# Performance work log

Measured on AMD Instinct MI355X. Metric: run time of the kernel, lower is better.

## Reference

```python
import jax, jax.numpy as jnp
import numpy as np

COMMITMENT = 1.0


def setup_inputs() -> dict:
    key = jax.random.key(0)
    k1, k2 = jax.random.split(key)
    input = jax.random.normal(k1, (8, 64, 64, 256), dtype=jnp.float32)
    embed = jax.random.normal(k2, (256, 8192), dtype=jnp.float32)  # [dim, n_embed]
    return {"input": input, "embed": embed}


def reference(input, embed):
    dim = embed.shape[0]
    flatten = input.reshape(-1, dim)  # [N, dim]
    dist = (
        jnp.sum(flatten * flatten, axis=1, keepdims=True)
        - 2.0 * (flatten @ embed)
        + jnp.sum(embed * embed, axis=0, keepdims=True)
    )
    embed_ind = jnp.argmin(dist, axis=1)  # == (-dist).max(1) indices
    embed_ind = embed_ind.reshape(input.shape[:-1])  # [B, H, W]
    quantize = jnp.take(embed.T, embed_ind, axis=0)  # codebook lookup [B,H,W,dim]
    loss = jnp.mean((jax.lax.stop_gradient(quantize) - input) ** 2) * COMMITMENT
    quantize = input + jax.lax.stop_gradient(quantize - input)  # straight-through
    return quantize, embed_ind, loss
```

## Files before the change

kernel.cpp:

```cpp
#include <hip/hip_runtime.h>
#include <hip/hip_fp16.h>

#define NROW 32768
#define DIM  256
#define NC   8192
#define CAP  16384
#define MARGINF 0.375f
#define BIAS 512.0f
#define AST 576
#define BST 576
#define LOSS_SCALE (1.0f / 8388608.0f)

typedef __attribute__((ext_vector_type(8))) _Float16 half8;
typedef __attribute__((ext_vector_type(4))) _Float16 half4;
typedef __attribute__((ext_vector_type(4))) float   floatx4;
typedef const __attribute__((address_space(1))) void* gas_p;
typedef __attribute__((address_space(3))) void*       las_p;

static __device__ __forceinline__ unsigned short f2hb(float f) {
    _Float16 h = (_Float16)f;
    unsigned short u;
    __builtin_memcpy(&u, &h, 2);
    return u;
}
static __device__ __forceinline__ unsigned umin_(unsigned a, unsigned b) { return a < b ? a : b; }
static __device__ __forceinline__ unsigned umax_(unsigned a, unsigned b) { return a > b ? a : b; }


__global__ void prep_a_k(const float* __restrict__ x, unsigned short* __restrict__ Ah,
                         float* __restrict__ norms) {
    int row  = blockIdx.x * 4 + (threadIdx.x >> 6);
    int lane = threadIdx.x & 63;
    const float4 v = ((const float4*)(x + (size_t)row * DIM))[lane];
    float s = v.x * v.x + v.y * v.y + v.z * v.z + v.w * v.w;
#pragma unroll
    for (int off = 32; off; off >>= 1) s += __shfl_down(s, off, 64);
    if (lane == 0) norms[row] = s;
    ushort4 hi4 = make_ushort4(f2hb(v.x), f2hb(v.y), f2hb(v.z), f2hb(v.w));
    ushort4 lo4 = make_ushort4(f2hb(v.x - (float)(_Float16)v.x),
                               f2hb(v.y - (float)(_Float16)v.y),
                               f2hb(v.z - (float)(_Float16)v.z),
                               f2hb(v.w - (float)(_Float16)v.w));
    unsigned short* rp = Ah + (size_t)row * AST;
    *(ushort4*)(rp + lane * 4)       = hi4;
    *(ushort4*)(rp + 288 + lane * 4) = lo4;
    if (lane < 8) {
        ushort4 ob = make_ushort4(0, 0, 0, 0);
        if (lane == 0) { ob.x = 0x3C00; ob.y = 0x3C00; }
        *(ushort4*)(rp + 256 + lane * 4) = ob;
    }
}

__global__ void code_norms_k(const float* __restrict__ e, unsigned short* __restrict__ Bh,
                             float* __restrict__ cHalf) {
    int j = blockIdx.x * 256 + threadIdx.x;
    float s = 0.f;
    for (int d = 0; d < DIM; ++d) { float v = e[(size_t)d * NC + j]; s += v * v; }
    cHalf[j] = 0.5f * s;
    float t = -0.5f * s - BIAS;
    unsigned short hi = f2hb(t);
    _Float16 hf; __builtin_memcpy(&hf, &hi, 2);
    unsigned short lo = f2hb(t - (float)hf);
    unsigned short* p = Bh + (size_t)j * BST + 256;
    p[0] = hi; p[1] = lo;
    for (int k2 = 2; k2 < 32; ++k2) p[k2] = 0;
}

__global__ void prep_b_k(const float* __restrict__ e, unsigned short* __restrict__ Bh) {
    __shared__ float t[32][33];
    int jb = blockIdx.x * 32, db = blockIdx.y * 32;
#pragma unroll
    for (int i = 0; i < 4; ++i)
        t[threadIdx.y + i * 8][threadIdx.x] =
            e[(size_t)(db + threadIdx.y + i * 8) * NC + jb + threadIdx.x];
    __syncthreads();
#pragma unroll
    for (int i = 0; i < 4; ++i) {
        int j = jb + threadIdx.y + i * 8;
        int d = db + threadIdx.x;
        float val = t[threadIdx.x][threadIdx.y + i * 8];
        Bh[(size_t)j * BST + d]       = f2hb(val);
        Bh[(size_t)j * BST + 288 + d] = f2hb(val - (float)(_Float16)val);
    }
}


__global__ __launch_bounds__(256, 1) void vq_cheap_k(
    const unsigned short* __restrict__ Ah, const unsigned short* __restrict__ Bh,
    const float* __restrict__ cHalf,
    float* __restrict__ pv, int* __restrict__ pj, float* __restrict__ psv)
{
    __shared__ __align__(16) _Float16 Asl[8][4096];
    __shared__ __align__(16) _Float16 Bsl[2][8192];
    __shared__ float chl[2048];

    const int tid  = threadIdx.x;
    const int js   = blockIdx.x & 3;
    const int rb   = blockIdx.x >> 2;
    const int row0 = rb * 128, col0 = js * 2048;
    const int lane = tid & 63, l15 = lane & 15, lq = lane >> 4;
    const int wave = tid >> 6;
    const int wr = (wave >> 1) * 64;
    const int wc = (wave & 1) * 128;
    const int sr = tid >> 2, sp = (tid & 3) * 8;

    const unsigned short* Abase = Ah + (size_t)(row0 + sr) * AST + sp;
#pragma unroll
    for (int c = 0; c < 8; ++c) {
        __builtin_amdgcn_global_load_lds((gas_p)(Abase + c * 32),            (las_p)&Asl[c][tid * 8],        16, 0, 0);
        __builtin_amdgcn_global_load_lds((gas_p)(Abase + 64 * AST + c * 32), (las_p)&Asl[c][2048 + tid * 8], 16, 0, 0);
    }
    {
        const float4* cp = (const float4*)(cHalf + col0);
        float4 a = cp[tid * 2], b = cp[tid * 2 + 1];
        a.x += BIAS; a.y += BIAS; a.z += BIAS; a.w += BIAS;
        b.x += BIAS; b.y += BIAS; b.z += BIAS; b.w += BIAS;
        ((float4*)chl)[tid * 2]     = a;
        ((float4*)chl)[tid * 2 + 1] = b;
    }

#define LOADB(JT_, C_, BUF_)                                                                  \
    do {                                                                                      \
        const unsigned short* bb_ = Bh + (size_t)(col0 + (JT_) * 256 + sr) * BST + (C_) * 32 + sp; \
        _Float16* lb_ = &Bsl[(BUF_)][tid * 8];                                                \
        __builtin_amdgcn_global_load_lds((gas_p)(bb_),             (las_p)lb_,           16, 0, 0); \
        __builtin_amdgcn_global_load_lds((gas_p)(bb_ + 64 * BST),  (las_p)(lb_ + 2048),  16, 0, 0); \
        __builtin_amdgcn_global_load_lds((gas_p)(bb_ + 128 * BST), (las_p)(lb_ + 4096),  16, 0, 0); \
        __builtin_amdgcn_global_load_lds((gas_p)(bb_ + 192 * BST), (las_p)(lb_ + 6144),  16, 0, 0); \
    } while (0)

    unsigned k1[16], k2[16];
#pragma unroll
    for (int s = 0; s < 16; ++s) { k1[s] = 0xFFFFFFFFu; k2[s] = 0xFFFFFFFFu; }

    const floatx4 fzero = {0.0f, 0.0f, 0.0f, 0.0f};
    floatx4 acc[4][8];
#pragma unroll
    for (int rf = 0; rf < 4; ++rf)
#pragma unroll
        for (int cf = 0; cf < 8; ++cf) acc[rf][cf] = fzero;

    LOADB(0, 0, 0);

    for (int jt = 0; jt < 8; ++jt) {
#pragma unroll
        for (int c = 0; c < 8; ++c) {
            const int buf = c & 1;
            __syncthreads();
            if (c < 7)           LOADB(jt, c + 1, buf ^ 1);
            else if (jt < 7)     LOADB(jt + 1, 0, buf ^ 1);

            half8 af[4], bf[8];
#pragma unroll
            for (int rf = 0; rf < 4; ++rf)
                af[rf] = *(const half8*)&Asl[c][(wr + rf * 16 + l15) * 32 + lq * 8];
#pragma unroll
            for (int cf = 0; cf < 8; ++cf)
                bf[cf] = *(const half8*)&Bsl[buf][(wc + cf * 16 + l15) * 32 + lq * 8];
#pragma unroll
            for (int rf = 0; rf < 4; ++rf)
#pragma unroll
                for (int cf = 0; cf < 8; ++cf)
                    acc[rf][cf] = __builtin_amdgcn_mfma_f32_16x16x32_f16(
                        af[rf], bf[cf], acc[rf][cf], 0, 0, 0);

            if (c == 7) {
#pragma unroll
                for (int cf = 0; cf < 8; ++cf) {
                    const unsigned colb = (unsigned)(jt * 256 + wc + cf * 16 + l15);
                    const float ch = chl[colb];
#pragma unroll
                    for (int rf = 0; rf < 4; ++rf)
#pragma unroll
                        for (int r = 0; r < 4; ++r) {
                            float s = acc[rf][cf][r] - ch;
                            unsigned key = (__float_as_uint(s) & 0xFFFFF800u) | colb;
                            int slot = rf * 4 + r;
                            unsigned t = umax_(key, k1[slot]);
                            k1[slot] = umin_(k1[slot], key);
                            k2[slot] = umin_(k2[slot], t);
                        }
                }
#pragma unroll
                for (int rf = 0; rf < 4; ++rf)
#pragma unroll
                    for (int cf = 0; cf < 8; ++cf) acc[rf][cf] = fzero;
            }
        }
    }
#undef LOADB

#pragma unroll
    for (int st = 1; st < 16; st <<= 1) {
#pragma unroll
        for (int s = 0; s < 16; ++s) {
            unsigned o1 = (unsigned)__shfl_xor((int)k1[s], st, 64);
            unsigned o2 = (unsigned)__shfl_xor((int)k2[s], st, 64);
            unsigned t = umax_(k1[s], o1);
            k1[s] = umin_(k1[s], o1);
            k2[s] = umin_(umin_(k2[s], o2), t);
        }
    }

    __syncthreads();
    unsigned* mk1 = (unsigned*)&Asl[0][0];
    unsigned* mk2 = (unsigned*)&Asl[1][0];
    if (l15 == 0) {
#pragma unroll
        for (int rf = 0; rf < 4; ++rf)
#pragma unroll
            for (int r = 0; r < 4; ++r) {
                int rloc = wr + rf * 16 + lq * 4 + r;
                int slot = rf * 4 + r;
                mk1[rloc * 2 + (wave & 1)] = k1[slot];
                mk2[rloc * 2 + (wave & 1)] = k2[slot];
            }
    }
    __syncthreads();
    if (tid < 128) {
        unsigned a1 = mk1[tid * 2], b1 = mk1[tid * 2 + 1];
        unsigned a2 = mk2[tid * 2], b2 = mk2[tid * 2 + 1];
        unsigned m1 = umin_(a1, b1);
        unsigned m2 = umin_(umin_(a2, b2), umax_(a1, b1));
        pv[(size_t)js * NROW + row0 + tid]  = __uint_as_float(m1 & 0xFFFFF800u);
        pj[(size_t)js * NROW + row0 + tid]  = (int)(m1 & 2047u) + js * 2048;
        psv[(size_t)js * NROW + row0 + tid] = __uint_as_float(m2 & 0xFFFFF800u);
    }
}


template<bool RESCUE>
static __device__ __forceinline__ void chunk_off(int c, int& ac, int& bc) {
    if constexpr (RESCUE) {
        if (c < 8)       { ac = c * 32;              bc = c * 32; }
        else if (c < 16) { ac = (c - 8) * 32;        bc = 288 + (c - 8) * 32; }
        else             { ac = 288 + (c - 16) * 32; bc = (c - 16) * 32; }
    } else {
        ac = c * 32; bc = c * 32;
    }
}

template<int CHUNKS, int JT, int JSB, bool RESCUE>
__global__ __launch_bounds__(256, 2) void vq_gemm_k(
    const unsigned short* __restrict__ Ah, const unsigned short* __restrict__ Bh,
    const float* __restrict__ cHalf,
    float* __restrict__ pv, int* __restrict__ pj, float* __restrict__ psv,
    const int* __restrict__ list, const int* __restrict__ cnt)
{
    __shared__ __align__(16) _Float16 As[2][4096];
    __shared__ __align__(16) _Float16 Bs[2][4096];

    const int tid  = threadIdx.x;
    const int js   = blockIdx.x & ((1 << JSB) - 1);
    const int rb   = blockIdx.x >> JSB;
    const int row0 = rb * 128, col0 = js * (JT * 128);
    const int lane = tid & 63, l15 = lane & 15, lq = lane >> 4;
    const int wave = tid >> 6;
    const int wrow = (wave >> 1) * 64, wcol = (wave & 1) * 64;
    const int sr = tid >> 2, sp = (tid & 3) * 8;

    int nact = 0;
    if constexpr (RESCUE) {
        nact = *cnt;
        if (row0 >= nact) return;
    }

    const unsigned short *Abase0, *Abase1;
    if constexpr (RESCUE) {
        int i0 = row0 + sr, i1 = i0 + 64;
        int r0 = (i0 < nact) ? list[i0] : 0;
        int r1 = (i1 < nact) ? list[i1] : 0;
        Abase0 = Ah + (size_t)r0 * AST + sp;
        Abase1 = Ah + (size_t)r1 * AST + sp;
    } else {
        Abase0 = Ah + (size_t)(row0 + sr) * AST + sp;
        Abase1 = Abase0 + 64 * AST;
    }

    unsigned k1[16], k2[16];
    float bvf[16]; int bjf[16];
#pragma unroll
    for (int s = 0; s < 16; ++s) {
        k1[s] = 0xFFFFFFFFu; k2[s] = 0xFFFFFFFFu;
        bvf[s] = -3.4e38f; bjf[s] = 0;
    }

    const floatx4 fzero = {0.0f, 0.0f, 0.0f, 0.0f};
    floatx4 acc[4][4];
#pragma unroll
    for (int rf = 0; rf < 4; ++rf)
#pragma unroll
        for (int cf = 0; cf < 4; ++cf) acc[rf][cf] = fzero;

    const unsigned short* Bb = Bh + (size_t)(col0 + sr) * BST + sp;

#define LOAD4(AC, BC, BUF, BBASE)                                                            \
    do {                                                                                     \
        _Float16* la_ = &As[(BUF)][tid * 8];                                                 \
        _Float16* lb_ = &Bs[(BUF)][tid * 8];                                                 \
        __builtin_amdgcn_global_load_lds((gas_p)(Abase0 + (AC)),            (las_p)la_,          16, 0, 0); \
        __builtin_amdgcn_global_load_lds((gas_p)(Abase1 + (AC)),            (las_p)(la_ + 2048), 16, 0, 0); \
        __builtin_amdgcn_global_load_lds((gas_p)((BBASE) + (BC)),           (las_p)lb_,          16, 0, 0); \
        __builtin_amdgcn_global_load_lds((gas_p)((BBASE) + 64 * BST + (BC)),(las_p)(lb_ + 2048), 16, 0, 0); \
    } while (0)

    LOAD4(0, 0, 0, Bb);

    for (int jt = 0; jt < JT; ++jt) {
        const int p = (CHUNKS & 1) ? (jt & 1) : 0;
#pragma unroll
        for (int c = 0; c < CHUNKS; ++c) {
            const int buf = (c & 1) ^ p;
            __syncthreads();
            if (c + 1 < CHUNKS) {
                int an, bn;
                chunk_off<RESCUE>(c + 1, an, bn);
                LOAD4(an, bn, buf ^ 1, Bb);
            } else if (jt + 1 < JT) {
                LOAD4(0, 0, buf ^ 1, Bb + 128 * BST);
            }

            half8 af[4], bf[4];
#pragma unroll
            for (int rf = 0; rf < 4; ++rf)
                af[rf] = *(const half8*)&As[buf][(wrow + rf * 16 + l15) * 32 + lq * 8];
#pragma unroll
            for (int cf = 0; cf < 4; ++cf)
                bf[cf] = *(const half8*)&Bs[buf][(wcol + cf * 16 + l15) * 32 + lq * 8];
#pragma unroll
            for (int rf = 0; rf < 4; ++rf)
#pragma unroll
                for (int cf = 0; cf < 4; ++cf)
                    acc[rf][cf] = __builtin_amdgcn_mfma_f32_16x16x32_f16(
                        af[rf], bf[cf], acc[rf][cf], 0, 0, 0);

            if (c == CHUNKS - 1) {
                if constexpr (RESCUE) {
                    const int colbase = col0 + jt * 128 + wcol;
#pragma unroll
                    for (int cf = 0; cf < 4; ++cf) {
                        const int col = colbase + cf * 16 + l15;
                        const float ch = cHalf[col];
#pragma unroll
                        for (int rf = 0; rf < 4; ++rf)
#pragma unroll
                            for (int r = 0; r < 4; ++r) {
                                float s = acc[rf][cf][r] - ch;
                                int slot = rf * 4 + r;
                                if (s > bvf[slot]) { bvf[slot] = s; bjf[slot] = col; }
                            }
                    }
                } else {
                    const unsigned colloc = (unsigned)(jt * 128 + wcol);
#pragma unroll
                    for (int cf = 0; cf < 4; ++cf) {
                        const unsigned colb = colloc + cf * 16 + l15;
#pragma unroll
                        for (int rf = 0; rf < 4; ++rf)
#pragma unroll
                            for (int r = 0; r < 4; ++r) {
                                unsigned key = (__float_as_uint(acc[rf][cf][r]) & 0xFFFFF800u) | colb;
                                int slot = rf * 4 + r;
                                unsigned t = umax_(key, k1[slot]);
                                k1[slot] = umin_(k1[slot], key);
                                k2[slot] = umin_(k2[slot], t);
                            }
                    }
                }
#pragma unroll
                for (int rf = 0; rf < 4; ++rf)
#pragma unroll
                    for (int cf = 0; cf < 4; ++cf) acc[rf][cf] = fzero;
            }
        }
        Bb += 128 * BST;
    }
#undef LOAD4

#pragma unroll
    for (int st = 1; st < 16; st <<= 1) {
#pragma unroll
        for (int s = 0; s < 16; ++s) {
            if constexpr (RESCUE) {
                float v2 = __shfl_xor(bvf[s], st, 64);
                int   j2 = __shfl_xor(bjf[s], st, 64);
                if (v2 > bvf[s] || (v2 == bvf[s] && j2 < bjf[s])) { bvf[s] = v2; bjf[s] = j2; }
            } else {
                unsigned o1 = (unsigned)__shfl_xor((int)k1[s], st, 64);
                unsigned o2 = (unsigned)__shfl_xor((int)k2[s], st, 64);
                unsigned t = umax_(k1[s], o1);
                k1[s] = umin_(k1[s], o1);
                k2[s] = umin_(umin_(k2[s], o2), t);
            }
        }
    }

    __syncthreads();
    if constexpr (RESCUE) {
        float* mv = (float*)&As[0][0];
        int*   mj = (int*)&Bs[0][0];
        if (l15 == 0) {
#pragma unroll
            for (int rf = 0; rf < 4; ++rf)
#pragma unroll
                for (int r = 0; r < 4; ++r) {
                    int rloc = wrow + rf * 16 + lq * 4 + r;
                    int slot = rf * 4 + r;
                    mv[rloc * 2 + (wave & 1)] = bvf[slot];
                    mj[rloc * 2 + (wave & 1)] = bjf[slot];
                }
        }
        __syncthreads();
        if (tid < 128) {
            float v0 = mv[tid * 2], v1 = mv[tid * 2 + 1];
            int   j0 = mj[tid * 2], j1 = mj[tid * 2 + 1];
            bool take1 = (v1 > v0) || (v1 == v0 && j1 < j0);
            pv[(size_t)js * CAP + row0 + tid] = take1 ? v1 : v0;
            pj[(size_t)js * CAP + row0 + tid] = take1 ? j1 : j0;
        }
    } else {
        unsigned* mk1 = (unsigned*)&As[0][0];
        unsigned* mk2 = (unsigned*)&Bs[0][0];
        if (l15 == 0) {
#pragma unroll
            for (int rf = 0; rf < 4; ++rf)
#pragma unroll
                for (int r = 0; r < 4; ++r) {
                    int rloc = wrow + rf * 16 + lq * 4 + r;
                    int slot = rf * 4 + r;
                    mk1[rloc * 2 + (wave & 1)] = k1[slot];
                    mk2[rloc * 2 + (wave & 1)] = k2[slot];
                }
        }
        __syncthreads();
        if (tid < 128) {
            unsigned a1 = mk1[tid * 2], b1 = mk1[tid * 2 + 1];
            unsigned a2 = mk2[tid * 2], b2 = mk2[tid * 2 + 1];
            unsigned m1 = umin_(a1, b1);
            unsigned m2 = umin_(umin_(a2, b2), umax_(a1, b1));
            pv[(size_t)js * NROW + row0 + tid] = __uint_as_float(m1 & 0xFFFFF800u);
            pj[(size_t)js * NROW + row0 + tid] = (int)(m1 & 2047u) + js * (JT * 128);
            psv[(size_t)js * NROW + row0 + tid] = __uint_as_float(m2 & 0xFFFFF800u);
        }
    }
}


__global__ void vq_reduce_k(const float* __restrict__ pv, const int* __restrict__ pj,
                            const float* __restrict__ psv,
                            const float* __restrict__ norms, const unsigned short* __restrict__ Bh,
                            float* __restrict__ qout, float* __restrict__ iout,
                            float* __restrict__ lout, int* __restrict__ list,
                            int* __restrict__ cnt)
{
    __shared__ int jbuf[64];
    const int row0 = blockIdx.x * 64;
    const int tid = threadIdx.x;
    if (tid < 64) {
        int row = row0 + tid;
        float bv = pv[row]; int bj = pj[row]; float sv = psv[row];
#pragma unroll
        for (int s = 1; s < 4; ++s) {
            float v = pv[(size_t)s * NROW + row];
            int   j = pj[(size_t)s * NROW + row];
            float s2 = psv[(size_t)s * NROW + row];
            bool better = (v > bv) || (v == bv && j < bj);
            float loseBest = better ? bv : v;
            sv = fmaxf(fmaxf(sv, s2), loseBest);
            if (better) { bv = v; bj = j; }
        }
        bool flagged = (bv - sv) < MARGINF;
        if (flagged) {
            int idx = atomicAdd(cnt, 1);
            if (idx < CAP) {
                list[idx] = row;
                jbuf[tid] = -1;
            } else {
                flagged = false;
            }
        }
        float rl = 0.f;
        if (!flagged) {
            iout[row] = (float)bj;
            jbuf[tid] = bj;
            rl = norms[row] - 2.0f * (bv + BIAS - 0.0625f);
        }
#pragma unroll
        for (int off = 32; off; off >>= 1) rl += __shfl_down(rl, off, 64);
        if (tid == 0) atomicAdd(lout, rl * LOSS_SCALE);
    }
    __syncthreads();
    const int lane = tid & 63;
    for (int r = tid >> 6; r < 64; r += 4) {
        int j = jbuf[r];
        if (j >= 0) {
            const _Float16* bp = (const _Float16*)Bh + (size_t)j * BST + lane * 4;
            half4 h = *(const half4*)bp;
            half4 l = *(const half4*)(bp + 288);
            float4 v;
            v.x = (float)h[0] + (float)l[0];
            v.y = (float)h[1] + (float)l[1];
            v.z = (float)h[2] + (float)l[2];
            v.w = (float)h[3] + (float)l[3];
            *(float4*)&qout[(size_t)(row0 + r) * DIM + lane * 4] = v;
        }
    }
}


__global__ void vq_reduce2_k(const float* __restrict__ pv2, const int* __restrict__ pj2,
                             const int* __restrict__ list, const int* __restrict__ cnt,
                             const float* __restrict__ norms, const unsigned short* __restrict__ Bh,
                             float* __restrict__ qout, float* __restrict__ iout,
                             float* __restrict__ lout)
{
    __shared__ int rbuf[64], jb2[64];
    const int n = *cnt < CAP ? *cnt : CAP;
    const int i0 = blockIdx.x * 64;
    if (i0 >= n) return;
    const int tid = threadIdx.x;
    if (tid < 64) {
        int i = i0 + tid;
        float rl = 0.f;
        if (i < n) {
            float bv = pv2[i]; int bj = pj2[i];
#pragma unroll 4
            for (int s = 1; s < 32; ++s) {
                float v = pv2[(size_t)s * CAP + i];
                int   j = pj2[(size_t)s * CAP + i];
                if (v > bv || (v == bv && j < bj)) { bv = v; bj = j; }
            }
            int row = list[i];
            iout[row] = (float)bj;
            rbuf[tid] = row;
            jb2[tid]  = bj;
            rl = norms[row] - 2.0f * bv;
        } else {
            rbuf[tid] = -1;
        }
#pragma unroll
        for (int off = 32; off; off >>= 1) rl += __shfl_down(rl, off, 64);
        if (tid == 0) atomicAdd(lout, rl * LOSS_SCALE);
    }
    __syncthreads();
    const int lane = tid & 63;
    for (int r = tid >> 6; r < 64; r += 4) {
        int row = rbuf[r];
        if (row >= 0) {
            const _Float16* bp = (const _Float16*)Bh + (size_t)jb2[r] * BST + lane * 4;
            half4 h = *(const half4*)bp;
            half4 l = *(const half4*)(bp + 288);
            float4 v;
            v.x = (float)h[0] + (float)l[0];
            v.y = (float)h[1] + (float)l[1];
            v.z = (float)h[2] + (float)l[2];
            v.w = (float)h[3] + (float)l[3];
            *(float4*)&qout[(size_t)row * DIM + lane * 4] = v;
        }
    }
}


__global__ void transpose_k(const float* __restrict__ e, float* __restrict__ eT) {
    __shared__ float t[32][33];
    int jb = blockIdx.x * 32, db = blockIdx.y * 32;
#pragma unroll
    for (int i = 0; i < 4; ++i)
        t[threadIdx.y + i * 8][threadIdx.x] =
            e[(size_t)(db + threadIdx.y + i * 8) * NC + jb + threadIdx.x];
    __syncthreads();
#pragma unroll
    for (int i = 0; i < 4; ++i)
        eT[(size_t)(jb + threadIdx.y + i * 8) * DIM + db + threadIdx.x] =
            t[threadIdx.x][threadIdx.y + i * 8];
}

__global__ void row_norms_k(const float* __restrict__ x, float* __restrict__ norms) {
    int row  = blockIdx.x * 4 + (threadIdx.x >> 6);
    int lane = threadIdx.x & 63;
    const float4 v = ((const float4*)(x + (size_t)row * DIM))[lane];
    float s = v.x * v.x + v.y * v.y + v.z * v.z + v.w * v.w;
#pragma unroll
    for (int off = 32; off; off >>= 1) s += __shfl_down(s, off, 64);
    if (lane == 0) norms[row] = s;
}

__global__ void code_norms_fb_k(const float* __restrict__ e, float* __restrict__ cHalf) {
    int j = blockIdx.x * 256 + threadIdx.x;
    float s = 0.f;
    for (int d = 0; d < DIM; ++d) { float v = e[(size_t)d * NC + j]; s += v * v; }
    cHalf[j] = 0.5f * s;
}

__global__ __launch_bounds__(256, 4) void vq_main_k(
    const float* __restrict__ x, const float* __restrict__ e,
    const float* __restrict__ eT, const float* __restrict__ norms,
    const float* __restrict__ cHalf, float* __restrict__ qout,
    float* __restrict__ iout, float* __restrict__ lout, int useT)
{
    __shared__ float  As[2][32 * 68];
    __shared__ float4 Bs[2][512];
    const int tid  = threadIdx.x;
    const int row0 = blockIdx.x * 64;
    const int ty = tid >> 4, tx = tid & 15;
    const int ar = tid >> 2, ak = (tid & 3) * 4;
    const int bk = tid >> 4, bj = tid & 15;
    float bestv[4]; int bestj[4];
#pragma unroll
    for (int i = 0; i < 4; ++i) { bestv[i] = -3.4e38f; bestj[i] = 0; }
    float acc[4][4];
    float4 pa0, pa1, pb0, pb1;
    {
        const float* xp = x + (size_t)(row0 + ar) * DIM + ak;
        pa0 = *(const float4*)xp;
        pa1 = *(const float4*)(xp + 16);
        const float* ep = e + (size_t)bk * NC + bj * 4;
        pb0 = *(const float4*)ep;
        pb1 = *(const float4*)(ep + 16 * NC);
    }
    int buf = 0;
    for (int c = 0; c < 1024; ++c) {
        const int kc = c & 7;
#pragma unroll
        for (int q = 0; q < 4; ++q) As[buf][(ak + q) * 68 + ar]      = ((const float*)&pa0)[q];
#pragma unroll
        for (int q = 0; q < 4; ++q) As[buf][(16 + ak + q) * 68 + ar] = ((const float*)&pa1)[q];
        Bs[buf][bk * 16 + bj]        = pb0;
        Bs[buf][(bk + 16) * 16 + bj] = pb1;
        __syncthreads();
        if (c + 1 < 1024) {
            int j0n  = ((c + 1) >> 3) * 64;
            int kk0n = ((c + 1) & 7) * 32;
            const float* xp = x + (size_t)(row0 + ar) * DIM + kk0n + ak;
            pa0 = *(const float4*)xp;
            pa1 = *(const float4*)(xp + 16);
            const float* ep = e + (size_t)(kk0n + bk) * NC + j0n + bj * 4;
            pb0 = *(const float4*)ep;
            pb1 = *(const float4*)(ep + 16 * NC);
        }
        if (kc == 0) {
#pragma unroll
            for (int i = 0; i < 4; ++i)
#pragma unroll
                for (int j = 0; j < 4; ++j) acc[i][j] = 0.f;
        }
#pragma unroll
        for (int k = 0; k < 32; ++k) {
            float4 a = *(const float4*)&As[buf][k * 68 + ty * 4];
            float4 b = *(const float4*)&Bs[buf][k * 16 + tx];
            acc[0][0] += a.x * b.x; acc[0][1] += a.x * b.y; acc[0][2] += a.x * b.z; acc[0][3] += a.x * b.w;
            acc[1][0] += a.y * b.x; acc[1][1] += a.y * b.y; acc[1][2] += a.y * b.z; acc[1][3] += a.y * b.w;
            acc[2][0] += a.z * b.x; acc[2][1] += a.z * b.y; acc[2][2] += a.z * b.z; acc[2][3] += a.z * b.w;
            acc[3][0] += a.w * b.x; acc[3][1] += a.w * b.y; acc[3][2] += a.w * b.z; acc[3][3] += a.w * b.w;
        }
        if (kc == 7) {
            int j0 = (c >> 3) * 64;
            float4 ch = *(const float4*)&cHalf[j0 + tx * 4];
            int jb0 = j0 + tx * 4;
#pragma unroll
            for (int i = 0; i < 4; ++i)
#pragma unroll
                for (int j = 0; j < 4; ++j) {
                    float s = acc[i][j] - ((const float*)&ch)[j];
                    if (s > bestv[i]) { bestv[i] = s; bestj[i] = jb0 + j; }
                }
        }
        buf ^= 1;
    }
    __syncthreads();
    float* redv   = &As[0][0];
    int*   redj   = (int*)&As[0][1024];
    int*   idxbuf = (int*)&As[1][0];
#pragma unroll
    for (int i = 0; i < 4; ++i) {
        int r = ty * 4 + i;
        redv[r * 16 + tx] = bestv[i];
        redj[r * 16 + tx] = bestj[i];
    }
    __syncthreads();
    if (tid < 64) {
        float bvv = redv[tid * 16];
        int   bj2 = redj[tid * 16];
#pragma unroll
        for (int t = 1; t < 16; ++t) {
            float v = redv[tid * 16 + t];
            int   j = redj[tid * 16 + t];
            if (v > bvv || (v == bvv && j < bj2)) { bvv = v; bj2 = j; }
        }
        iout[row0 + tid] = (float)bj2;
        idxbuf[tid] = bj2;
        float rl = norms[row0 + tid] - 2.0f * bvv;
#pragma unroll
        for (int off = 32; off; off >>= 1) rl += __shfl_down(rl, off, 64);
        if (tid == 0) atomicAdd(lout, rl * LOSS_SCALE);
    }
    __syncthreads();
    {
        const int rr = tid >> 6, lane = tid & 63;
        for (int r = rr; r < 64; r += 4) {
            int j = idxbuf[r];
            float4 v;
            if (useT) {
                v = *(const float4*)&eT[(size_t)j * DIM + lane * 4];
            } else {
                int d = lane * 4;
                v.x = e[(size_t)d * NC + j];
                v.y = e[(size_t)(d + 1) * NC + j];
                v.z = e[(size_t)(d + 2) * NC + j];
                v.w = e[(size_t)(d + 3) * NC + j];
            }
            *(float4*)&qout[(size_t)(row0 + r) * DIM + lane * 4] = v;
        }
    }
}


extern "C" void kernel_launch(void* const* d_in, const int* in_sizes, int n_in,
                              void* d_out, int out_size, void* d_ws, size_t ws_size,
                              hipStream_t stream) {
    const float* x = (const float*)d_in[0];
    const float* e = (const float*)d_in[1];

    float* qout = (float*)d_out;
    float* iout = qout + (size_t)NROW * DIM;
    float* lout = iout + NROW;

    char* ws = (char*)d_ws;
    const size_t offAh    = 0;
    const size_t offBh    = offAh + 37748736;
    const size_t offNorms = offBh + 9437184;
    const size_t offCH    = offNorms + 131072;
    const size_t offPV    = offCH + 32768;
    const size_t offPJ    = offPV + 524288;
    const size_t offPSV   = offPJ + 524288;
    const size_t offPV2   = offPSV + 524288;
    const size_t offPJ2   = offPV2 + 2097152;
    const size_t offList  = offPJ2 + 2097152;
    const size_t offCnt   = offList + 65536;
    const size_t needFast = offCnt + 256;

    hipMemsetAsync(lout, 0, sizeof(float), stream);

    if (ws_size >= needFast) {
        unsigned short* Ah = (unsigned short*)(ws + offAh);
        unsigned short* Bh = (unsigned short*)(ws + offBh);
        float* norms = (float*)(ws + offNorms);
        float* cHalf = (float*)(ws + offCH);
        float* pv    = (float*)(ws + offPV);
        int*   pj    = (int*)(ws + offPJ);
        float* psv   = (float*)(ws + offPSV);
        float* pv2   = (float*)(ws + offPV2);
        int*   pj2   = (int*)(ws + offPJ2);
        int*   list  = (int*)(ws + offList);
        int*   cnt   = (int*)(ws + offCnt);

        hipMemsetAsync(cnt, 0, sizeof(int), stream);
        prep_a_k<<<NROW / 4, 256, 0, stream>>>(x, Ah, norms);
        code_norms_k<<<NC / 256, 256, 0, stream>>>(e, Bh, cHalf);
        prep_b_k<<<dim3(NC / 32, DIM / 32), dim3(32, 8), 0, stream>>>(e, Bh);
        vq_cheap_k<<<1024, 256, 0, stream>>>(Ah, Bh, cHalf, pv, pj, psv);
        vq_reduce_k<<<NROW / 64, 256, 0, stream>>>(
            pv, pj, psv, norms, Bh, qout, iout, lout, list, cnt);
        vq_gemm_k<24, 2, 5, true><<<(CAP / 128) * 32, 256, 0, stream>>>(
            Ah, Bh, cHalf, pv2, pj2, nullptr, list, cnt);
        vq_reduce2_k<<<CAP / 64, 256, 0, stream>>>(
            pv2, pj2, list, cnt, norms, Bh, qout, iout, lout);
    } else {
        float* fws   = (float*)d_ws;
        float* norms = fws;
        float* cHalf = fws + NROW;
        float* eT    = fws + NROW + NC;
        size_t need_T = (size_t)(NROW + NC) * sizeof(float) + (size_t)NC * DIM * sizeof(float);
        int useT = (ws_size >= need_T) ? 1 : 0;
        row_norms_k<<<NROW / 4, 256, 0, stream>>>(x, norms);
        code_norms_fb_k<<<NC / 256, 256, 0, stream>>>(e, cHalf);
        if (useT)
            transpose_k<<<dim3(NC / 32, DIM / 32), dim3(32, 8), 0, stream>>>(e, eT);
        vq_main_k<<<NROW / 64, 256, 0, stream>>>(x, e, eT, norms, cHalf, qout, iout, lout, useT);
    }
}
```

Measured before the change: 419.5 us.

## Use 8-wave blocks with swizzled LDS layout in cheap VQ GEMM and tighten margin

```diff
diff --git a/kernel.cpp b/kernel.cpp
--- a/kernel.cpp
+++ b/kernel.cpp
@@ -5,7 +5,7 @@
 #define DIM  256
 #define NC   8192
 #define CAP  16384
-#define MARGINF 0.375f
+#define MARGINF 0.25f
 #define BIAS 512.0f
 #define AST 576
 #define BST 576
@@ -85,7 +85,7 @@
 }
 
 
-__global__ __launch_bounds__(256, 1) void vq_cheap_k(
+__global__ __launch_bounds__(512, 2) void vq_cheap_k(
     const unsigned short* __restrict__ Ah, const unsigned short* __restrict__ Bh,
     const float* __restrict__ cHalf,
     float* __restrict__ pv, int* __restrict__ pj, float* __restrict__ psv)
@@ -100,33 +100,27 @@
     const int row0 = rb * 128, col0 = js * 2048;
     const int lane = tid & 63, l15 = lane & 15, lq = lane >> 4;
     const int wave = tid >> 6;
-    const int wr = (wave >> 1) * 64;
-    const int wc = (wave & 1) * 128;
-    const int sr = tid >> 2, sp = (tid & 3) * 8;
-
-    const unsigned short* Abase = Ah + (size_t)(row0 + sr) * AST + sp;
-#pragma unroll
-    for (int c = 0; c < 8; ++c) {
-        __builtin_amdgcn_global_load_lds((gas_p)(Abase + c * 32),            (las_p)&Asl[c][tid * 8],        16, 0, 0);
-        __builtin_amdgcn_global_load_lds((gas_p)(Abase + 64 * AST + c * 32), (las_p)&Asl[c][2048 + tid * 8], 16, 0, 0);
-    }
+    const int wr = (wave >> 2) * 64;
+    const int wc = (wave & 3) * 64;
+    const int sr = tid >> 2;
+    const int ks = (((tid & 3) ^ (sr & 3) ^ ((sr >> 2) & 3))) * 8;
+
+    const unsigned short* Abase = Ah + (size_t)(row0 + sr) * AST + ks;
+#pragma unroll
+    for (int c = 0; c < 8; ++c)
+        __builtin_amdgcn_global_load_lds((gas_p)(Abase + c * 32), (las_p)&Asl[c][tid * 8], 16, 0, 0);
     {
-        const float4* cp = (const float4*)(cHalf + col0);
-        float4 a = cp[tid * 2], b = cp[tid * 2 + 1];
+        float4 a = ((const float4*)(cHalf + col0))[tid];
         a.x += BIAS; a.y += BIAS; a.z += BIAS; a.w += BIAS;
-        b.x += BIAS; b.y += BIAS; b.z += BIAS; b.w += BIAS;
-        ((float4*)chl)[tid * 2]     = a;
-        ((float4*)chl)[tid * 2 + 1] = b;
+        ((float4*)chl)[tid] = a;
     }
 
 #define LOADB(JT_, C_, BUF_)                                                                  \
     do {                                                                                      \
-        const unsigned short* bb_ = Bh + (size_t)(col0 + (JT_) * 256 + sr) * BST + (C_) * 32 + sp; \
+        const unsigned short* bb_ = Bh + (size_t)(col0 + (JT_) * 256 + sr) * BST + (C_) * 32 + ks; \
         _Float16* lb_ = &Bsl[(BUF_)][tid * 8];                                                \
-        __builtin_amdgcn_global_load_lds((gas_p)(bb_),             (las_p)lb_,           16, 0, 0); \
-        __builtin_amdgcn_global_load_lds((gas_p)(bb_ + 64 * BST),  (las_p)(lb_ + 2048),  16, 0, 0); \
-        __builtin_amdgcn_global_load_lds((gas_p)(bb_ + 128 * BST), (las_p)(lb_ + 4096),  16, 0, 0); \
-        __builtin_amdgcn_global_load_lds((gas_p)(bb_ + 192 * BST), (las_p)(lb_ + 6144),  16, 0, 0); \
+        __builtin_amdgcn_global_load_lds((gas_p)bb_,               (las_p)lb_,          16, 0, 0); \
+        __builtin_amdgcn_global_load_lds((gas_p)(bb_ + 128 * BST), (las_p)(lb_ + 4096), 16, 0, 0); \
     } while (0)
 
     unsigned k1[16], k2[16];
@@ -134,11 +128,11 @@
     for (int s = 0; s < 16; ++s) { k1[s] = 0xFFFFFFFFu; k2[s] = 0xFFFFFFFFu; }
 
     const floatx4 fzero = {0.0f, 0.0f, 0.0f, 0.0f};
-    floatx4 acc[4][8];
+    floatx4 acc[4][4];
 #pragma unroll
     for (int rf = 0; rf < 4; ++rf)
 #pragma unroll
-        for (int cf = 0; cf < 8; ++cf) acc[rf][cf] = fzero;
+        for (int cf = 0; cf < 4; ++cf) acc[rf][cf] = fzero;
 
     LOADB(0, 0, 0);
 
@@ -150,23 +144,29 @@
             if (c < 7)           LOADB(jt, c + 1, buf ^ 1);
             else if (jt < 7)     LOADB(jt + 1, 0, buf ^ 1);
 
-            half8 af[4], bf[8];
+            half8 af[4], bf[4];
+#pragma unroll
+            for (int rf = 0; rf < 4; ++rf) {
+                const int m = wr + rf * 16 + l15;
+                const int g = lq ^ (m & 3) ^ ((m >> 2) & 3);
+                af[rf] = *(const half8*)&Asl[c][m * 32 + g * 8];
+            }
+#pragma unroll
+            for (int cf = 0; cf < 4; ++cf) {
+                const int n = wc + cf * 16 + l15;
+                const int g = lq ^ (n & 3) ^ ((n >> 2) & 3);
+                bf[cf] = *(const half8*)&Bsl[buf][n * 32 + g * 8];
+            }
 #pragma unroll
             for (int rf = 0; rf < 4; ++rf)
-                af[rf] = *(const half8*)&Asl[c][(wr + rf * 16 + l15) * 32 + lq * 8];
-#pragma unroll
-            for (int cf = 0; cf < 8; ++cf)
-                bf[cf] = *(const half8*)&Bsl[buf][(wc + cf * 16 + l15) * 32 + lq * 8];
-#pragma unroll
-            for (int rf = 0; rf < 4; ++rf)
-#pragma unroll
-                for (int cf = 0; cf < 8; ++cf)
+#pragma unroll
+                for (int cf = 0; cf < 4; ++cf)
                     acc[rf][cf] = __builtin_amdgcn_mfma_f32_16x16x32_f16(
                         af[rf], bf[cf], acc[rf][cf], 0, 0, 0);
 
             if (c == 7) {
 #pragma unroll
-                for (int cf = 0; cf < 8; ++cf) {
+                for (int cf = 0; cf < 4; ++cf) {
                     const unsigned colb = (unsigned)(jt * 256 + wc + cf * 16 + l15);
                     const float ch = chl[colb];
 #pragma unroll
@@ -184,7 +184,7 @@
 #pragma unroll
                 for (int rf = 0; rf < 4; ++rf)
 #pragma unroll
-                    for (int cf = 0; cf < 8; ++cf) acc[rf][cf] = fzero;
+                    for (int cf = 0; cf < 4; ++cf) acc[rf][cf] = fzero;
             }
         }
     }
@@ -212,16 +212,19 @@
             for (int r = 0; r < 4; ++r) {
                 int rloc = wr + rf * 16 + lq * 4 + r;
                 int slot = rf * 4 + r;
-                mk1[rloc * 2 + (wave & 1)] = k1[slot];
-                mk2[rloc * 2 + (wave & 1)] = k2[slot];
+                mk1[rloc * 4 + (wave & 3)] = k1[slot];
+                mk2[rloc * 4 + (wave & 3)] = k2[slot];
             }
     }
     __syncthreads();
     if (tid < 128) {
-        unsigned a1 = mk1[tid * 2], b1 = mk1[tid * 2 + 1];
-        unsigned a2 = mk2[tid * 2], b2 = mk2[tid * 2 + 1];
-        unsigned m1 = umin_(a1, b1);
-        unsigned m2 = umin_(umin_(a2, b2), umax_(a1, b1));
+        unsigned a0 = mk1[tid * 4], a1 = mk1[tid * 4 + 1], a2 = mk1[tid * 4 + 2], a3 = mk1[tid * 4 + 3];
+        unsigned x = umin_(a0, a1), y = umax_(a0, a1);
+        unsigned z = umin_(a2, a3), w = umax_(a2, a3);
+        unsigned m1  = umin_(x, z);
+        unsigned sm1 = umin_(umax_(x, z), umin_(y, w));
+        unsigned s0 = mk2[tid * 4], s1 = mk2[tid * 4 + 1], s2 = mk2[tid * 4 + 2], s3 = mk2[tid * 4 + 3];
+        unsigned m2 = umin_(umin_(umin_(s0, s1), umin_(s2, s3)), sm1);
         pv[(size_t)js * NROW + row0 + tid]  = __uint_as_float(m1 & 0xFFFFF800u);
         pj[(size_t)js * NROW + row0 + tid]  = (int)(m1 & 2047u) + js * 2048;
         psv[(size_t)js * NROW + row0 + tid] = __uint_as_float(m2 & 0xFFFFF800u);
@@ -758,7 +761,7 @@
         prep_a_k<<<NROW / 4, 256, 0, stream>>>(x, Ah, norms);
         code_norms_k<<<NC / 256, 256, 0, stream>>>(e, Bh, cHalf);
         prep_b_k<<<dim3(NC / 32, DIM / 32), dim3(32, 8), 0, stream>>>(e, Bh);
-        vq_cheap_k<<<1024, 256, 0, stream>>>(Ah, Bh, cHalf, pv, pj, psv);
+        vq_cheap_k<<<1024, 512, 0, stream>>>(Ah, Bh, cHalf, pv, pj, psv);
         vq_reduce_k<<<NROW / 64, 256, 0, stream>>>(
             pv, pj, psv, norms, Bh, qout, iout, lout, list, cnt);
         vq_gemm_k<24, 2, 5, true><<<(CAP / 128) * 32, 256, 0, stream>>>(
```

After: 362.3 us. 1.16x faster.
